# Kernel optimization log

Hardware: AMD Instinct MI355X
Metric: run time of the kernel (lower is better)

## Reference

```python
import jax, jax.numpy as jnp
import numpy as np

N_OBJ, N_REL = 5000, 20000
HID, POOL, N_RELCLS, N_OBJCLS = 512, 4096, 51, 151


def setup_inputs() -> dict:
    key = jax.random.key(0)
    ks = jax.random.split(key, 8)
    s = lambda fi, fo: (2.0 / (fi + fo)) ** 0.5  # xavier-ish scale
    return {
        'edge_ctx': jax.random.normal(ks[0], (N_OBJ, HID), jnp.float32),
        'union_features': jax.random.normal(ks[1], (N_REL, POOL), jnp.float32),
        'W_pe': jax.random.normal(ks[2], (2 * HID, HID), jnp.float32) * (10.0 * (1.0 / HID) ** 0.5),
        'b_pe': jnp.zeros((2 * HID,), jnp.float32),
        'W_pc': jax.random.normal(ks[3], (POOL, 2 * HID), jnp.float32) * s(2 * HID, POOL),
        'b_pc': jnp.zeros((POOL,), jnp.float32),
        'W_cc': jax.random.normal(ks[4], (N_RELCLS, POOL), jnp.float32) * s(POOL, N_RELCLS),
        'b_cc': jnp.zeros((N_RELCLS,), jnp.float32),
        'freq_emb': jax.random.normal(ks[5], (N_OBJCLS * N_OBJCLS, N_RELCLS), jnp.float32) * 0.1,
        'obj_preds': jax.random.randint(ks[6], (N_OBJ,), 0, N_OBJCLS, jnp.int64 if jax.config.jax_enable_x64 else jnp.int32),
        'pair_idx': jax.random.randint(ks[7], (N_REL, 2), 0, N_OBJ, jnp.int64 if jax.config.jax_enable_x64 else jnp.int32),
    }


def reference(edge_ctx, union_features, W_pe, b_pe, W_pc, b_pc, W_cc, b_cc,
              freq_emb, obj_preds, pair_idx):
    # post_emb -> relu -> split into head/tail halves ([N,2,HID] view)
    edge_rep = jax.nn.relu(edge_ctx @ W_pe.T + b_pe)          # [N, 2*HID]
    head_rep, tail_rep = edge_rep[:, :HID], edge_rep[:, HID:]

    hi, ti = pair_idx[:, 0], pair_idx[:, 1]
    prod = jnp.concatenate([head_rep[hi], tail_rep[ti]], axis=-1)  # [R, 2*HID]
    prod_rep = prod @ W_pc.T + b_pc                               # [R, POOL]

    ctx_dists = (prod_rep * union_features) @ W_cc.T + b_cc      # [R, 51]

    # frequency bias: embedding lookup at head_cls * num_obj_cls + tail_cls
    pair_lbl = obj_preds[hi] * N_OBJCLS + obj_preds[ti]
    frq_dists = freq_emb[pair_lbl]                               # [R, 51]
    # dropout p=0.3 is identity in eval mode
    return ctx_dists + frq_dists
```

## Files before the change

kernel.cpp:

```cpp
#include <hip/hip_runtime.h>

typedef unsigned short u16;
typedef unsigned int u32;
typedef __attribute__((ext_vector_type(4))) float f32x4;
typedef __attribute__((ext_vector_type(8))) __bf16 bf16x8;
typedef __attribute__((ext_vector_type(8))) u16 u16x8;

__device__ __forceinline__ u16 f2bf(float x) {
  u32 u = __float_as_uint(x);
  u32 r = (u + 0x7FFFu + ((u >> 16) & 1u)) >> 16;
  return (u16)r;
}

__device__ __forceinline__ float bf2f(u16 b) {
  return __uint_as_float((u32)b << 16);
}

__device__ __forceinline__ void gl16(const void* g, void* l) {
  auto* gp = (__attribute__((address_space(1))) u32*)(g);
  auto* lp = (__attribute__((address_space(3))) u32*)(l);
  __builtin_amdgcn_global_load_lds(gp, lp, 16, 0, 0);
}

__device__ __forceinline__ f32x4 mfma16(bf16x8 a, bf16x8 b, f32x4 c) {
  return __builtin_amdgcn_mfma_f32_16x16x32_bf16(a, b, c, 0, 0, 0);
}

__device__ __forceinline__ u16x8 cvt8(const float* p) {
  float4 a = *(const float4*)p, b = *(const float4*)(p + 4);
  u16x8 v;
  v[0] = f2bf(a.x); v[1] = f2bf(a.y); v[2] = f2bf(a.z); v[3] = f2bf(a.w);
  v[4] = f2bf(b.x); v[5] = f2bf(b.y); v[6] = f2bf(b.z); v[7] = f2bf(b.w);
  return v;
}

__global__ void k_prep(const float* __restrict__ ec, const float* __restrict__ wpe,
                       const float* __restrict__ wpc, const float* __restrict__ wcc,
                       u16* __restrict__ ecb, u16* __restrict__ wpeb,
                       u16* __restrict__ wpcb, u16* __restrict__ wccb) {
  int i = blockIdx.x * 256 + threadIdx.x;
  if (i < 320000) {
    *(u16x8*)(ecb + (long)i * 8) = cvt8(ec + (long)i * 8);
  } else if (i < 385536) {
    int j = i - 320000;
    *(u16x8*)(wpeb + (long)j * 8) = cvt8(wpe + (long)j * 8);
  } else if (i < 909824) {
    int j = i - 385536;
    *(u16x8*)(wpcb + (long)j * 8) = cvt8(wpc + (long)j * 8);
  } else if (i < 942592) {
    int j = i - 909824;
    long base = (long)j * 8;
    int row = (int)(base >> 12);
    int col = (int)(base & 4095);
    u16x8 v;
    if (row < 51) {
      v = cvt8(wcc + (long)row * 4096 + col);
    } else {
#pragma unroll
      for (int k = 0; k < 8; ++k) v[k] = 0;
    }
    *(u16x8*)(wccb + base) = v;
  }
}

__device__ __forceinline__ void cstep(const char* sA, const char* sB,
                                      const int (&aOff)[4], const int (&bOff)[4],
                                      f32x4 (&acc)[4][4]) {
  bf16x8 af[4], bv[4];
#pragma unroll
  for (int mi = 0; mi < 4; ++mi) af[mi] = *(const bf16x8*)(sA + aOff[mi]);
#pragma unroll
  for (int ni = 0; ni < 4; ++ni) bv[ni] = *(const bf16x8*)(sB + bOff[ni]);
  __builtin_amdgcn_s_setprio(1);
#pragma unroll
  for (int mi = 0; mi < 4; ++mi)
#pragma unroll
    for (int ni = 0; ni < 4; ++ni)
      acc[mi][ni] = mfma16(af[mi], bv[ni], acc[mi][ni]);
  __builtin_amdgcn_s_setprio(0);
}

__device__ __forceinline__ void cstep64(const char* buf,
                                        const int (&aOff)[4][2], const int (&bOff)[4][2],
                                        f32x4 (&acc)[4][4]) {
  bf16x8 af[4][2], bv[4][2];
#pragma unroll
  for (int mi = 0; mi < 4; ++mi)
#pragma unroll
    for (int ks = 0; ks < 2; ++ks) af[mi][ks] = *(const bf16x8*)(buf + aOff[mi][ks]);
#pragma unroll
  for (int ni = 0; ni < 4; ++ni)
#pragma unroll
    for (int ks = 0; ks < 2; ++ks) bv[ni][ks] = *(const bf16x8*)(buf + bOff[ni][ks]);
  __builtin_amdgcn_s_setprio(1);
#pragma unroll
  for (int ks = 0; ks < 2; ++ks)
#pragma unroll
    for (int mi = 0; mi < 4; ++mi)
#pragma unroll
      for (int ni = 0; ni < 4; ++ni)
        acc[mi][ni] = mfma16(af[mi][ks], bv[ni][ks], acc[mi][ni]);
  __builtin_amdgcn_s_setprio(0);
}

__global__ __launch_bounds__(256, 2) void k_gemm1(const u16* __restrict__ A, const u16* __restrict__ B,
                                                  const float* __restrict__ bias, u16* __restrict__ outp) {
  __shared__ char lds[65536];
  int bx = blockIdx.x;
  int rb = bx >> 3, nb = bx & 7;
  int rowBase = rb * 128, nBase = nb * 128;
  int t = threadIdx.x, lane = t & 63, wid = t >> 6;
  int wr = wid >> 1, wc = wid & 1, lm = lane & 15, lg = lane >> 4;
  int ar0 = t >> 2, ar1 = 64 + ar0, c4 = t & 3;
  int sw0 = (c4 * 16) ^ (((ar0 >> 1) & 3) << 4);
  int sw1 = (c4 * 16) ^ (((ar1 >> 1) & 3) << 4);
  const char* aS0 = (const char*)(A + (long)min(rowBase + ar0, 4999) * 512) + sw0;
  const char* aS1 = (const char*)(A + (long)min(rowBase + ar1, 4999) * 512) + sw1;
  const char* bS0 = (const char*)(B + (long)(nBase + ar0) * 512) + sw0;
  const char* bS1 = (const char*)(B + (long)(nBase + ar1) * 512) + sw1;
  int t16 = t * 16;
  int aOff[4], bOff[4];
#pragma unroll
  for (int mi = 0; mi < 4; ++mi) { int r = wr * 64 + mi * 16 + lm; aOff[mi] = r * 64 + ((lg * 16) ^ (((r >> 1) & 3) << 4)); }
#pragma unroll
  for (int ni = 0; ni < 4; ++ni) { int r = wc * 64 + ni * 16 + lm; bOff[ni] = r * 64 + ((lg * 16) ^ (((r >> 1) & 3) << 4)); }
  f32x4 acc[4][4] = {};

#define STAGE_G(k, sb) do { \
    gl16(aS0 + (k) * 2, (sb) + t16); gl16(aS1 + (k) * 2, (sb) + 4096 + t16); \
    gl16(bS0 + (k) * 2, (sb) + 8192 + t16); gl16(bS1 + (k) * 2, (sb) + 12288 + t16); \
  } while (0)

  STAGE_G(0, lds);
  STAGE_G(32, lds + 16384);
  STAGE_G(64, lds + 32768);

  int cur = 0, stg = 3;
  for (int kt = 0; kt < 16; ++kt) {
    if (kt < 13) {
      char* sb = lds + stg * 16384;
      STAGE_G((kt + 3) * 32, sb);
    }
    if (kt < 13)       asm volatile("s_waitcnt vmcnt(12)" ::: "memory");
    else if (kt == 13) asm volatile("s_waitcnt vmcnt(8)" ::: "memory");
    else if (kt == 14) asm volatile("s_waitcnt vmcnt(4)" ::: "memory");
    else               asm volatile("s_waitcnt vmcnt(0)" ::: "memory");
    __builtin_amdgcn_s_barrier();
    char* cb = lds + cur * 16384;
    cstep(cb, cb + 8192, aOff, bOff, acc);
    __builtin_amdgcn_s_barrier();
    cur = (cur == 3) ? 0 : cur + 1;
    stg = (stg == 3) ? 0 : stg + 1;
  }
#undef STAGE_G

#pragma unroll
  for (int mi = 0; mi < 4; ++mi)
#pragma unroll
    for (int ni = 0; ni < 4; ++ni) {
      int n = nBase + wc * 64 + ni * 16 + lm;
      float bvv = bias[n];
#pragma unroll
      for (int rg = 0; rg < 4; ++rg) {
        int r = rowBase + wr * 64 + mi * 16 + lg * 4 + rg;
        if (r < 5000) {
          float v = acc[mi][ni][rg] + bvv;
          v = v > 0.f ? v : 0.f;
          outp[(long)r * 1024 + n] = f2bf(v);
        }
      }
    }
}

__global__ __launch_bounds__(256, 2) void k_gemm2(const u16* __restrict__ erep, const u16* __restrict__ wpc,
                                                  const float* __restrict__ bpc, u16* __restrict__ Hout,
                                                  u16* __restrict__ Tout) {
  __shared__ char lds[65536];
  int bx = blockIdx.x;
  int h = (bx >= 1280) ? 1 : 0;
  int rr = bx - h * 1280;
  int rb = rr >> 5, nb = rr & 31;
  int rowBase = rb * 128, nBase = nb * 128;
  u16* outp = h ? Tout : Hout;
  int t = threadIdx.x, lane = t & 63, wid = t >> 6;
  int wr = wid >> 1, wc = wid & 1, lm = lane & 15, lg = lane >> 4;
  int ar = t >> 3, c8 = t & 7;
  int srcswz = ((c8 ^ (ar & 7)) << 4);
  const char* aP[4];
  const char* bP[4];
#pragma unroll
  for (int i = 0; i < 4; ++i) {
    int Ra = min(rowBase + i * 32 + ar, 4999);
    aP[i] = (const char*)(erep + (long)Ra * 1024 + h * 512) + srcswz;
    int Rb = nBase + i * 32 + ar;
    bP[i] = (const char*)(wpc + (long)Rb * 1024 + h * 512) + srcswz;
  }
  int t16 = t * 16;
  int aOff[4][2], bOff[4][2];
#pragma unroll
  for (int mi = 0; mi < 4; ++mi)
#pragma unroll
    for (int ks = 0; ks < 2; ++ks) {
      int r = wr * 64 + mi * 16 + lm;
      aOff[mi][ks] = r * 128 + (((ks * 4 + lg) ^ (r & 7)) << 4);
    }
#pragma unroll
  for (int ni = 0; ni < 4; ++ni)
#pragma unroll
    for (int ks = 0; ks < 2; ++ks) {
      int r = wc * 64 + ni * 16 + lm;
      bOff[ni][ks] = 16384 + r * 128 + (((ks * 4 + lg) ^ (r & 7)) << 4);
    }
  f32x4 acc[4][4] = {};

#define STAGE2(kk, buf) do { \
    _Pragma("unroll") \
    for (int i = 0; i < 4; ++i) { \
      gl16(aP[i] + (kk) * 2, (buf) + i * 4096 + t16); \
      gl16(bP[i] + (kk) * 2, (buf) + 16384 + i * 4096 + t16); \
    } \
  } while (0)

  STAGE2(0, lds);
  for (int kt = 0; kt < 8; ++kt) {
    if (kt < 7) STAGE2((kt + 1) * 64, lds + (((kt + 1) & 1) ? 32768 : 0));
    if (kt < 7) asm volatile("s_waitcnt vmcnt(8)" ::: "memory");
    else        asm volatile("s_waitcnt vmcnt(0)" ::: "memory");
    __builtin_amdgcn_s_barrier();
    cstep64(lds + ((kt & 1) ? 32768 : 0), aOff, bOff, acc);
    __builtin_amdgcn_s_barrier();
  }
#undef STAGE2

#pragma unroll
  for (int mi = 0; mi < 4; ++mi)
#pragma unroll
    for (int ni = 0; ni < 4; ++ni) {
      int n = nBase + wc * 64 + ni * 16 + lm;
      float bvv = h ? 0.f : bpc[n];
#pragma unroll
      for (int rg = 0; rg < 4; ++rg) {
        int r = rowBase + wr * 64 + mi * 16 + lg * 4 + rg;
        if (r < 5000) {
          float v = acc[mi][ni][rg] + bvv;
          outp[(long)r * 4096 + n] = f2bf(v);
        }
      }
    }
}

__global__ __launch_bounds__(256) void k_final(
    const u16* __restrict__ H, const u16* __restrict__ T,
    const u16* __restrict__ wcc,
    const float* __restrict__ un,
    const float* __restrict__ bcc, const float* __restrict__ freq,
    const int* __restrict__ preds, const int* __restrict__ pidx,
    float* __restrict__ outp) {
  __shared__ char sU[32768];
  __shared__ int sLbl[128];
  int bx = blockIdx.x;
  int rb = bx >> 3, ps = bx & 7;
  int rowBase = rb * 128;
  int t = threadIdx.x, lane = t & 63, wid = t >> 6;
  int lm = lane & 15, lg = lane >> 4;
  int r16 = t >> 4, c16 = t & 15;

  if (t < 128) {
    int rG = min(rowBase + t, 19999);
    sLbl[t] = preds[pidx[2 * rG]] * 151 + preds[pidx[2 * rG + 1]];
  }

  u32 hoff[8], toff[8], uoff[8];
#pragma unroll
  for (int p = 0; p < 8; ++p) {
    int rG = min(rowBase + p * 16 + r16, 19999);
    hoff[p] = (u32)pidx[2 * rG] * 8192u + (u32)c16 * 16u;
    toff[p] = (u32)pidx[2 * rG + 1] * 8192u + (u32)c16 * 16u;
    uoff[p] = (u32)rG * 16384u + (u32)c16 * 32u;
  }
  const char* Hc = (const char*)H;
  const char* Tc = (const char*)T;
  const char* Uc = (const char*)un;
  int pc0 = ps * 512;

  f32x4 outAcc[2][4] = {};

  for (int chk = 0; chk < 4; ++chk) {
    int pcBase = pc0 + chk * 128;
    if (chk) __syncthreads();
#pragma unroll
    for (int p = 0; p < 8; ++p) {
      int r = p * 16 + r16;
      u16x8 h8 = *(const u16x8*)(Hc + hoff[p] + (u32)pcBase * 2u);
      u16x8 t8 = *(const u16x8*)(Tc + toff[p] + (u32)pcBase * 2u);
      float4 u0 = *(const float4*)(Uc + uoff[p] + (u32)pcBase * 4u);
      float4 u1 = *(const float4*)(Uc + uoff[p] + (u32)pcBase * 4u + 16u);
      float uu[8];
      *(float4*)(uu) = u0;
      *(float4*)(uu + 4) = u1;
      u16x8 pv;
#pragma unroll
      for (int j = 0; j < 8; ++j)
        pv[j] = f2bf((bf2f(h8[j]) + bf2f(t8[j])) * uu[j]);
      *(u16x8*)(sU + r * 256 + ((c16 * 16) ^ ((r & 7) << 4))) = pv;
    }
    __syncthreads();

#pragma unroll
    for (int kb = 0; kb < 4; ++kb) {
      bf16x8 aU[2], bW[4];
#pragma unroll
      for (int m2 = 0; m2 < 2; ++m2) {
        int r = wid * 32 + m2 * 16 + lm;
        aU[m2] = *(const bf16x8*)(sU + r * 256 + ((kb * 64 + lg * 16) ^ ((r & 7) << 4)));
      }
#pragma unroll
      for (int ni = 0; ni < 4; ++ni)
        bW[ni] = *(const bf16x8*)(wcc + (long)(ni * 16 + lm) * 4096 + pcBase + kb * 32 + lg * 8);
      __builtin_amdgcn_s_setprio(1);
#pragma unroll
      for (int m2 = 0; m2 < 2; ++m2)
#pragma unroll
        for (int ni = 0; ni < 4; ++ni)
          outAcc[m2][ni] = mfma16(aU[m2], bW[ni], outAcc[m2][ni]);
      __builtin_amdgcn_s_setprio(0);
    }
  }

#pragma unroll
  for (int m2 = 0; m2 < 2; ++m2)
#pragma unroll
    for (int rg = 0; rg < 4; ++rg) {
      int r = wid * 32 + m2 * 16 + lg * 4 + rg;
      int rG = rowBase + r;
      if (rG < 20000) {
#pragma unroll
        for (int ni = 0; ni < 4; ++ni) {
          int c = ni * 16 + lm;
          if (c < 51) {
            float v = outAcc[m2][ni][rg];
            if (ps == 0) v += bcc[c] + freq[(long)sLbl[r] * 51 + c];
            atomicAdd(&outp[(long)rG * 51 + c], v);
          }
        }
      }
    }
}

extern "C" void kernel_launch(void* const* d_in, const int* in_sizes, int n_in,
                              void* d_out, int out_size, void* d_ws, size_t ws_size,
                              hipStream_t stream) {
  const float* edge_ctx = (const float*)d_in[0];
  const float* unionf   = (const float*)d_in[1];
  const float* W_pe     = (const float*)d_in[2];
  const float* b_pe     = (const float*)d_in[3];
  const float* W_pc     = (const float*)d_in[4];
  const float* b_pc     = (const float*)d_in[5];
  const float* W_cc     = (const float*)d_in[6];
  const float* b_cc     = (const float*)d_in[7];
  const float* freq     = (const float*)d_in[8];
  const int*   preds    = (const int*)d_in[9];
  const int*   pidx     = (const int*)d_in[10];
  float* out = (float*)d_out;
  char* ws = (char*)d_ws;

  u16* Hb   = (u16*)(ws + 0);
  u16* Tb   = (u16*)(ws + 40960000);
  u16* erep = (u16*)(ws + 81920000);
  u16* wpcb = (u16*)(ws + 92160000);
  u16* wccb = (u16*)(ws + 100548608);
  u16* ecb  = (u16*)(ws + 101072896);
  u16* wpeb = (u16*)(ws + 106192896);

  hipMemsetAsync(d_out, 0, (size_t)out_size * 4, stream);
  k_prep<<<3682, 256, 0, stream>>>(edge_ctx, W_pe, W_pc, W_cc, ecb, wpeb, wpcb, wccb);
  k_gemm1<<<320, 256, 0, stream>>>(ecb, wpeb, b_pe, erep);
  k_gemm2<<<2560, 256, 0, stream>>>(erep, wpcb, b_pc, Hb, Tb);
  k_final<<<1256, 256, 0, stream>>>(Hb, Tb, wccb, unionf, b_cc, freq, preds, pidx, out);
}
```

Baseline: 263.4 us.

## Replace atomic split-K accumulation with partial buffer and separate reduction kernel

The final kernel now handles 64-row tiles instead of 128, doubling the grid so more blocks are in flight. Each pool slice writes its partial 51-wide result to a workspace buffer instead of issuing atomicAdds into the output. A new reduction kernel sums the eight partials and adds the bias and frequency-embedding lookup. This also drops the output memset, but adds an extra launch and extra partial-buffer traffic.

```diff
diff --git a/kernel.cpp b/kernel.cpp
--- a/kernel.cpp
+++ b/kernel.cpp
@@ -253,26 +253,19 @@
     const u16* __restrict__ H, const u16* __restrict__ T,
     const u16* __restrict__ wcc,
     const float* __restrict__ un,
-    const float* __restrict__ bcc, const float* __restrict__ freq,
-    const int* __restrict__ preds, const int* __restrict__ pidx,
-    float* __restrict__ outp) {
-  __shared__ char sU[32768];
-  __shared__ int sLbl[128];
+    const int* __restrict__ pidx,
+    float* __restrict__ partial) {
+  __shared__ char sU[16384];
   int bx = blockIdx.x;
   int rb = bx >> 3, ps = bx & 7;
-  int rowBase = rb * 128;
+  int rowBase = rb * 64;
   int t = threadIdx.x, lane = t & 63, wid = t >> 6;
   int lm = lane & 15, lg = lane >> 4;
   int r16 = t >> 4, c16 = t & 15;
 
-  if (t < 128) {
-    int rG = min(rowBase + t, 19999);
-    sLbl[t] = preds[pidx[2 * rG]] * 151 + preds[pidx[2 * rG + 1]];
-  }
-
-  u32 hoff[8], toff[8], uoff[8];
-#pragma unroll
-  for (int p = 0; p < 8; ++p) {
+  u32 hoff[4], toff[4], uoff[4];
+#pragma unroll
+  for (int p = 0; p < 4; ++p) {
     int rG = min(rowBase + p * 16 + r16, 19999);
     hoff[p] = (u32)pidx[2 * rG] * 8192u + (u32)c16 * 16u;
     toff[p] = (u32)pidx[2 * rG + 1] * 8192u + (u32)c16 * 16u;
@@ -283,13 +276,13 @@
   const char* Uc = (const char*)un;
   int pc0 = ps * 512;
 
-  f32x4 outAcc[2][4] = {};
+  f32x4 outAcc[4] = {};
 
   for (int chk = 0; chk < 4; ++chk) {
     int pcBase = pc0 + chk * 128;
     if (chk) __syncthreads();
 #pragma unroll
-    for (int p = 0; p < 8; ++p) {
+    for (int p = 0; p < 4; ++p) {
       int r = p * 16 + r16;
       u16x8 h8 = *(const u16x8*)(Hc + hoff[p] + (u32)pcBase * 2u);
       u16x8 t8 = *(const u16x8*)(Tc + toff[p] + (u32)pcBase * 2u);
@@ -308,43 +301,47 @@
 
 #pragma unroll
     for (int kb = 0; kb < 4; ++kb) {
-      bf16x8 aU[2], bW[4];
-#pragma unroll
-      for (int m2 = 0; m2 < 2; ++m2) {
-        int r = wid * 32 + m2 * 16 + lm;
-        aU[m2] = *(const bf16x8*)(sU + r * 256 + ((kb * 64 + lg * 16) ^ ((r & 7) << 4)));
-      }
+      int r = wid * 16 + lm;
+      bf16x8 aU = *(const bf16x8*)(sU + r * 256 + ((kb * 64 + lg * 16) ^ ((r & 7) << 4)));
+      bf16x8 bW[4];
 #pragma unroll
       for (int ni = 0; ni < 4; ++ni)
         bW[ni] = *(const bf16x8*)(wcc + (long)(ni * 16 + lm) * 4096 + pcBase + kb * 32 + lg * 8);
       __builtin_amdgcn_s_setprio(1);
 #pragma unroll
-      for (int m2 = 0; m2 < 2; ++m2)
-#pragma unroll
-        for (int ni = 0; ni < 4; ++ni)
-          outAcc[m2][ni] = mfma16(aU[m2], bW[ni], outAcc[m2][ni]);
+      for (int ni = 0; ni < 4; ++ni)
+        outAcc[ni] = mfma16(aU, bW[ni], outAcc[ni]);
       __builtin_amdgcn_s_setprio(0);
     }
   }
 
 #pragma unroll
-  for (int m2 = 0; m2 < 2; ++m2)
-#pragma unroll
-    for (int rg = 0; rg < 4; ++rg) {
-      int r = wid * 32 + m2 * 16 + lg * 4 + rg;
-      int rG = rowBase + r;
-      if (rG < 20000) {
-#pragma unroll
-        for (int ni = 0; ni < 4; ++ni) {
-          int c = ni * 16 + lm;
-          if (c < 51) {
-            float v = outAcc[m2][ni][rg];
-            if (ps == 0) v += bcc[c] + freq[(long)sLbl[r] * 51 + c];
-            atomicAdd(&outp[(long)rG * 51 + c], v);
-          }
-        }
+  for (int rg = 0; rg < 4; ++rg) {
+    int r = wid * 16 + lg * 4 + rg;
+    int rG = rowBase + r;
+    if (rG < 20000) {
+      long base = ((long)ps * 20000 + rG) * 64;
+#pragma unroll
+      for (int ni = 0; ni < 4; ++ni) {
+        int c = ni * 16 + lm;
+        if (c < 51) partial[base + c] = outAcc[ni][rg];
       }
     }
+  }
+}
+
+__global__ void k_red(const float* __restrict__ partial, const float* __restrict__ bcc,
+                      const float* __restrict__ freq, const int* __restrict__ preds,
+                      const int* __restrict__ pidx, float* __restrict__ outp) {
+  int idx = blockIdx.x * 256 + threadIdx.x;
+  if (idx >= 20000 * 64) return;
+  int row = idx >> 6, c = idx & 63;
+  if (c >= 51) return;
+  float s = 0.f;
+#pragma unroll
+  for (int i = 0; i < 8; ++i) s += partial[((long)i * 20000 + row) * 64 + c];
+  int lbl = preds[pidx[2 * row]] * 151 + preds[pidx[2 * row + 1]];
+  outp[(long)row * 51 + c] = s + bcc[c] + freq[(long)lbl * 51 + c];
 }
 
 extern "C" void kernel_launch(void* const* d_in, const int* in_sizes, int n_in,
@@ -364,17 +361,18 @@
   float* out = (float*)d_out;
   char* ws = (char*)d_ws;
 
-  u16* Hb   = (u16*)(ws + 0);
-  u16* Tb   = (u16*)(ws + 40960000);
-  u16* erep = (u16*)(ws + 81920000);
-  u16* wpcb = (u16*)(ws + 92160000);
-  u16* wccb = (u16*)(ws + 100548608);
-  u16* ecb  = (u16*)(ws + 101072896);
-  u16* wpeb = (u16*)(ws + 106192896);
-
-  hipMemsetAsync(d_out, 0, (size_t)out_size * 4, stream);
+  u16* Hb    = (u16*)(ws + 0);
+  u16* Tb    = (u16*)(ws + 40960000);
+  u16* erep  = (u16*)(ws + 81920000);
+  u16* wpcb  = (u16*)(ws + 92160000);
+  u16* wccb  = (u16*)(ws + 100548608);
+  u16* ecb   = (u16*)(ws + 101072896);
+  u16* wpeb  = (u16*)(ws + 106192896);
+  float* par = (float*)(ws + 107241472);
+
   k_prep<<<3682, 256, 0, stream>>>(edge_ctx, W_pe, W_pc, W_cc, ecb, wpeb, wpcb, wccb);
   k_gemm1<<<320, 256, 0, stream>>>(ecb, wpeb, b_pe, erep);
   k_gemm2<<<2560, 256, 0, stream>>>(erep, wpcb, b_pc, Hb, Tb);
-  k_final<<<1256, 256, 0, stream>>>(Hb, Tb, wccb, unionf, b_cc, freq, preds, pidx, out);
-}
+  k_final<<<2504, 256, 0, stream>>>(Hb, Tb, wccb, unionf, pidx, par);
+  k_red<<<5000, 256, 0, stream>>>(par, b_cc, freq, preds, pidx, out);
+}
```

Result: no change. 263.9 us (+0.2%).
